# Performance work log

Hardware: AMD Instinct MI355X
Metric: run time of the kernel (lower is better)

## Reference

```python
import jax, jax.numpy as jnp
import numpy as np

B, S, HID = 2, 2048, 2048
H, G = 16, 1
D = HID // H  # 128


def setup_inputs() -> dict:
    key = jax.random.key(0)
    ks = jax.random.split(key, 10)
    sc = 0.02
    inp = {
        "hidden_states": jax.random.normal(ks[0], (B, S, HID), jnp.float32),
        # 1 above the diagonal -> masked out (matches torch code: scores += mask * -1e9)
        "causal_mask": jnp.triu(jnp.ones((1, 1, S, S), jnp.float32), k=1),
        "padding_mask": jnp.zeros((B, S), jnp.float32),
        "Wq": jax.random.normal(ks[1], (HID, HID), jnp.float32) * sc,
        "bq": jnp.zeros((HID,), jnp.float32),
        "Wk": jax.random.normal(ks[2], (G * D, HID), jnp.float32) * sc,
        "bk": jnp.zeros((G * D,), jnp.float32),
        "Wv": jax.random.normal(ks[3], (G * D, HID), jnp.float32) * sc,
        "bv": jnp.zeros((G * D,), jnp.float32),
        "Wo": jax.random.normal(ks[4], (HID, HID), jnp.float32) * sc,
        "bo": jnp.zeros((HID,), jnp.float32),
    }
    return inp


def reference(hidden_states, causal_mask, padding_mask, Wq, bq, Wk, bk, Wv, bv, Wo, bo):
    b, s, _ = hidden_states.shape
    q = hidden_states @ Wq.T + bq            # [B,S,HID]
    k = hidden_states @ Wk.T + bk            # [B,S,G*D]
    v = hidden_states @ Wv.T + bv            # [B,S,G*D]
    q = q.reshape(b, s, H, D).transpose(0, 2, 1, 3)   # [B,H,S,D]
    k = k.reshape(b, s, G, D).transpose(0, 2, 1, 3)   # [B,G,S,D]
    v = v.reshape(b, s, G, D).transpose(0, 2, 1, 3)   # [B,G,S,D]
    # broadcast G=1 KV heads against H query heads (exactly what torch.matmul does)
    scores = jnp.matmul(q, jnp.swapaxes(k, -1, -2)) / jnp.sqrt(jnp.float32(D))  # [B,H,S,S]
    scores = scores + causal_mask * (-1e9)
    scores = scores + padding_mask[:, None, None, :] * (-1e9)
    weights = jax.nn.softmax(scores, axis=-1)
    out = jnp.matmul(weights, v)                       # [B,H,S,D]
    out = out.transpose(0, 2, 1, 3).reshape(b, s, H * D)
    return out @ Wo.T + bo
```

## Files before the change

kernel.cpp:

```cpp
#include <hip/hip_runtime.h>
#include <hip/hip_bf16.h>

typedef __attribute__((ext_vector_type(8))) short s8v;
typedef __attribute__((ext_vector_type(4))) float f4v;
typedef __hip_bfloat16 bf16;

#define S_LEN 2048
#define HID_DIM 2048
#define N_HEADS 16
#define HEAD_D 128
#define M_ROWS 4096
#define N_FUSED 2304

#define EXP2F(x) __builtin_amdgcn_exp2f(x)

static __device__ inline short f2b_bits(float f) {
  bf16 h = __float2bfloat16(f);
  short u;
  __builtin_memcpy(&u, &h, 2);
  return u;
}
static __device__ inline unsigned pk_bf16(float a, float b) {
  __hip_bfloat162 h2 = __float22bfloat162_rn(float2{a, b});
  unsigned u;
  __builtin_memcpy(&u, &h2, 4);
  return u;
}

struct Cvt5 {
  const float* src[5];
  bf16* dst[5];
  long n8[5];
};

__global__ __launch_bounds__(256) void cvt_f32_bf16(Cvt5 c) {
  long i = (long)blockIdx.x * 256 + threadIdx.x;
#pragma unroll
  for (int s = 0; s < 5; ++s) {
    long n8 = c.n8[s];
    if (i < n8) {
      const float* p = c.src[s] + i * 8;
      float4 f0 = *(const float4*)p;
      float4 f1 = *(const float4*)(p + 4);
      s8v t;
      t[0] = f2b_bits(f0.x); t[1] = f2b_bits(f0.y);
      t[2] = f2b_bits(f0.z); t[3] = f2b_bits(f0.w);
      t[4] = f2b_bits(f1.x); t[5] = f2b_bits(f1.y);
      t[6] = f2b_bits(f1.z); t[7] = f2b_bits(f1.w);
      *(s8v*)(c.dst[s] + i * 8) = t;
      return;
    }
    i -= n8;
  }
}

__global__ __launch_bounds__(256) void gemm_qkv(
    const bf16* __restrict__ A, const bf16* __restrict__ Wf,
    const float* __restrict__ bq, const float* __restrict__ bk,
    const float* __restrict__ bv,
    bf16* __restrict__ qout, bf16* __restrict__ kout, bf16* __restrict__ vtout) {
  __shared__ __align__(16) bf16 As[128 * 72];
  __shared__ __align__(16) bf16 Bs[128 * 72];
  const int t = threadIdx.x;
  const int lane = t & 63, wid = t >> 6;
  const int l15 = lane & 15, quad = lane >> 4;
  const int wm = wid >> 1, wn = wid & 1;
  const int bm = blockIdx.x, bn = blockIdx.y;
  f4v acc[4][4] = {};
  for (int kt = 0; kt < HID_DIM / 64; ++kt) {
    __syncthreads();
#pragma unroll
    for (int i = 0; i < 4; ++i) {
      int idx = t + i * 256;
      int row = idx >> 3, c8 = (idx & 7) * 8;
      *(uint4*)&As[row * 72 + c8] =
          *(const uint4*)&A[(size_t)(bm * 128 + row) * HID_DIM + kt * 64 + c8];
      *(uint4*)&Bs[row * 72 + c8] =
          *(const uint4*)&Wf[(size_t)(bn * 128 + row) * HID_DIM + kt * 64 + c8];
    }
    __syncthreads();
#pragma unroll
    for (int ks = 0; ks < 2; ++ks) {
      s8v af[4], bfr[4];
#pragma unroll
      for (int mi = 0; mi < 4; ++mi)
        af[mi] = *(const s8v*)&As[(wm * 64 + mi * 16 + l15) * 72 + ks * 32 + quad * 8];
#pragma unroll
      for (int ni = 0; ni < 4; ++ni)
        bfr[ni] = *(const s8v*)&Bs[(wn * 64 + ni * 16 + l15) * 72 + ks * 32 + quad * 8];
#pragma unroll
      for (int mi = 0; mi < 4; ++mi)
#pragma unroll
        for (int ni = 0; ni < 4; ++ni)
          acc[mi][ni] = __builtin_amdgcn_mfma_f32_16x16x32_bf16(af[mi], bfr[ni], acc[mi][ni], 0, 0, 0);
    }
  }
  if (bn < 16) {
#pragma unroll
    for (int ni = 0; ni < 4; ++ni) {
      int cl = wn * 64 + ni * 16 + l15;
      float bvv = bq[bn * 128 + cl];
#pragma unroll
      for (int mi = 0; mi < 4; ++mi)
#pragma unroll
        for (int r = 0; r < 4; ++r) {
          int row = bm * 128 + wm * 64 + mi * 16 + quad * 4 + r;
          qout[(size_t)row * HID_DIM + bn * 128 + cl] = __float2bfloat16(acc[mi][ni][r] + bvv);
        }
    }
  } else if (bn == 16) {
#pragma unroll
    for (int ni = 0; ni < 4; ++ni) {
      int cl = wn * 64 + ni * 16 + l15;
      float bvv = bk[cl];
#pragma unroll
      for (int mi = 0; mi < 4; ++mi)
#pragma unroll
        for (int r = 0; r < 4; ++r) {
          int row = bm * 128 + wm * 64 + mi * 16 + quad * 4 + r;
          kout[(size_t)row * HEAD_D + cl] = __float2bfloat16(acc[mi][ni][r] + bvv);
        }
    }
  } else {
#pragma unroll
    for (int ni = 0; ni < 4; ++ni) {
      int cl = wn * 64 + ni * 16 + l15;
      float bvv = bv[cl];
#pragma unroll
      for (int mi = 0; mi < 4; ++mi)
#pragma unroll
        for (int r = 0; r < 4; ++r) {
          int row = bm * 128 + wm * 64 + mi * 16 + quad * 4 + r;
          vtout[(size_t)cl * M_ROWS + row] = __float2bfloat16(acc[mi][ni][r] + bvv);
        }
    }
  }
}

template <bool WBF>
__global__ __launch_bounds__(256) void gemm_o(
    const bf16* __restrict__ A, const void* __restrict__ Wp,
    const float* __restrict__ bias, float* __restrict__ C) {
  __shared__ __align__(16) bf16 As[128 * 72];
  __shared__ __align__(16) bf16 Bs[128 * 72];
  const int t = threadIdx.x;
  const int lane = t & 63, wid = t >> 6;
  const int l15 = lane & 15, quad = lane >> 4;
  const int wm = wid >> 1, wn = wid & 1;
  const int bm = blockIdx.x, bn = blockIdx.y;
  f4v acc[4][4] = {};
  for (int kt = 0; kt < HID_DIM / 64; ++kt) {
    __syncthreads();
#pragma unroll
    for (int i = 0; i < 4; ++i) {
      int idx = t + i * 256;
      int row = idx >> 3, c8 = (idx & 7) * 8;
      *(uint4*)&As[row * 72 + c8] =
          *(const uint4*)&A[(size_t)(bm * 128 + row) * HID_DIM + kt * 64 + c8];
      if constexpr (WBF) {
        *(uint4*)&Bs[row * 72 + c8] =
            *(const uint4*)&((const bf16*)Wp)[(size_t)(bn * 128 + row) * HID_DIM + kt * 64 + c8];
      } else {
        const float* s = (const float*)Wp + (size_t)(bn * 128 + row) * HID_DIM + kt * 64 + c8;
        float4 f0 = *(const float4*)s;
        float4 f1 = *(const float4*)(s + 4);
        s8v tmp;
        tmp[0] = f2b_bits(f0.x); tmp[1] = f2b_bits(f0.y);
        tmp[2] = f2b_bits(f0.z); tmp[3] = f2b_bits(f0.w);
        tmp[4] = f2b_bits(f1.x); tmp[5] = f2b_bits(f1.y);
        tmp[6] = f2b_bits(f1.z); tmp[7] = f2b_bits(f1.w);
        *(s8v*)&Bs[row * 72 + c8] = tmp;
      }
    }
    __syncthreads();
#pragma unroll
    for (int ks = 0; ks < 2; ++ks) {
      s8v af[4], bfr[4];
#pragma unroll
      for (int mi = 0; mi < 4; ++mi)
        af[mi] = *(const s8v*)&As[(wm * 64 + mi * 16 + l15) * 72 + ks * 32 + quad * 8];
#pragma unroll
      for (int ni = 0; ni < 4; ++ni)
        bfr[ni] = *(const s8v*)&Bs[(wn * 64 + ni * 16 + l15) * 72 + ks * 32 + quad * 8];
#pragma unroll
      for (int mi = 0; mi < 4; ++mi)
#pragma unroll
        for (int ni = 0; ni < 4; ++ni)
          acc[mi][ni] = __builtin_amdgcn_mfma_f32_16x16x32_bf16(af[mi], bfr[ni], acc[mi][ni], 0, 0, 0);
    }
  }
#pragma unroll
  for (int ni = 0; ni < 4; ++ni) {
    int col = bn * 128 + wn * 64 + ni * 16 + l15;
    float bvv = bias[col];
#pragma unroll
    for (int mi = 0; mi < 4; ++mi)
#pragma unroll
      for (int r = 0; r < 4; ++r) {
        int row = bm * 128 + wm * 64 + mi * 16 + quad * 4 + r;
        C[(size_t)row * HID_DIM + col] = acc[mi][ni][r] + bvv;
      }
  }
}

__global__ __launch_bounds__(256, 2) void attn_fwd(
    const bf16* q, const bf16* __restrict__ k, const bf16* __restrict__ vt,
    bf16* o) {
  constexpr int FS = 528;
  __shared__ __align__(16) bf16 KsF[16 * FS];
  __shared__ __align__(16) bf16 VtF[16 * FS];
  __shared__ __align__(16) bf16 PsF[16 * FS];
  const int t = threadIdx.x;
  const int lane = t & 63, w = t >> 6;
  const int l15 = lane & 15, quad = lane >> 4;
  const int u = blockIdx.x >> 1, b = blockIdx.x & 1;
  const int c = (u < 128) ? (255 - 2 * u) : (2 * (u - 128));
  const size_t bs = (size_t)b * S_LEN;
  const int row0 = c * 8;

  s8v qf[2][4];
#pragma unroll
  for (int mi = 0; mi < 2; ++mi)
#pragma unroll
    for (int ks = 0; ks < 4; ++ks)
      qf[mi][ks] = *(const s8v*)&q[(bs + row0 + (l15 & 7)) * HID_DIM +
                                   (w * 4 + mi * 2 + (l15 >> 3)) * HEAD_D + ks * 32 + quad * 8];

  float mst[2] = {-1e30f, -1e30f};
  float lst[2] = {0.f, 0.f};
  f4v acco[2][8] = {};
  const float scale2 = 0.12754245f;
  const int jt = (c >> 3) + 1;

  uint4 kreg[4], vreg[4];
#pragma unroll
  for (int i = 0; i < 4; ++i) {
    int idx = t + i * 256;
    kreg[i] = *(const uint4*)&k[(bs + (idx >> 4)) * HEAD_D + (idx & 15) * 8];
    vreg[i] = *(const uint4*)&vt[(size_t)(idx >> 3) * M_ROWS + bs + (idx & 7) * 8];
  }

  for (int j = 0; j < jt; ++j) {
    __syncthreads();
#pragma unroll
    for (int i = 0; i < 4; ++i) {
      int idx = t + i * 256;
      int krow = idx >> 4, kc = idx & 15;
      *(uint4*)&KsF[(((krow >> 4) << 2) | (kc >> 2)) * FS + ((krow & 15) << 5) + ((kc & 3) << 3)] = kreg[i];
      int vd = idx >> 3, vc = idx & 7;
      *(uint4*)&VtF[(((vd >> 4) << 1) | (vc >> 2)) * FS + ((vd & 15) << 5) + ((vc & 3) << 3)] = vreg[i];
    }
    if (j + 1 < jt) {
#pragma unroll
      for (int i = 0; i < 4; ++i) {
        int idx = t + i * 256;
        kreg[i] = *(const uint4*)&k[(bs + (j + 1) * 64 + (idx >> 4)) * HEAD_D + (idx & 15) * 8];
        vreg[i] = *(const uint4*)&vt[(size_t)(idx >> 3) * M_ROWS + bs + (j + 1) * 64 + (idx & 7) * 8];
      }
    }
    __syncthreads();

    f4v accs[4][2] = {};
#pragma unroll
    for (int ks = 0; ks < 4; ++ks) {
      s8v kf[4];
#pragma unroll
      for (int ni = 0; ni < 4; ++ni)
        kf[ni] = *(const s8v*)&KsF[(ni * 4 + ks) * FS + l15 * 32 + quad * 8];
#pragma unroll
      for (int ni = 0; ni < 4; ++ni)
#pragma unroll
        for (int mi = 0; mi < 2; ++mi)
          accs[ni][mi] = __builtin_amdgcn_mfma_f32_16x16x32_bf16(kf[ni], qf[mi][ks], accs[ni][mi], 0, 0, 0);
    }

#pragma unroll
    for (int mi = 0; mi < 2; ++mi) {
      const int mg = row0 + (l15 & 7);
      const bool full = (j * 64 + 63 <= row0);
      float tmax = -1e30f;
#pragma unroll
      for (int ni = 0; ni < 4; ++ni)
#pragma unroll
        for (int r = 0; r < 4; ++r) {
          int ng = j * 64 + ni * 16 + quad * 4 + r;
          float s = accs[ni][mi][r];
          if (!full && ng > mg) s = -1e30f;
          accs[ni][mi][r] = s;
          tmax = fmaxf(tmax, s);
        }
      tmax = fmaxf(tmax, __shfl_xor(tmax, 16, 64));
      tmax = fmaxf(tmax, __shfl_xor(tmax, 32, 64));
      float mnew = fmaxf(mst[mi], tmax);
      float nms = -mnew * scale2;
      float alpha = EXP2F(fmaf(mst[mi], scale2, nms));
      float psum = 0.f;
#pragma unroll
      for (int ni = 0; ni < 4; ++ni) {
        float p0 = EXP2F(fmaf(accs[ni][mi][0], scale2, nms));
        float p1 = EXP2F(fmaf(accs[ni][mi][1], scale2, nms));
        float p2 = EXP2F(fmaf(accs[ni][mi][2], scale2, nms));
        float p3 = EXP2F(fmaf(accs[ni][mi][3], scale2, nms));
        psum += (p0 + p1) + (p2 + p3);
        uint2 packed;
        packed.x = pk_bf16(p0, p1);
        packed.y = pk_bf16(p2, p3);
        *(uint2*)&PsF[(w * 4 + mi * 2 + (ni >> 1)) * FS + l15 * 32 + (ni & 1) * 16 + quad * 4] = packed;
      }
      psum += __shfl_xor(psum, 16, 64);
      psum += __shfl_xor(psum, 32, 64);
      lst[mi] = lst[mi] * alpha + psum;
      mst[mi] = mnew;
#pragma unroll
      for (int r = 0; r < 4; ++r) {
        float ar = __shfl(alpha, quad * 4 + r, 64);
#pragma unroll
        for (int di = 0; di < 8; ++di) acco[mi][di][r] *= ar;
      }
    }

#pragma unroll
    for (int ks = 0; ks < 2; ++ks) {
      s8v pf[2], vf[8];
#pragma unroll
      for (int mi = 0; mi < 2; ++mi)
        pf[mi] = *(const s8v*)&PsF[(w * 4 + mi * 2 + ks) * FS + l15 * 32 + quad * 8];
#pragma unroll
      for (int di = 0; di < 8; ++di)
        vf[di] = *(const s8v*)&VtF[(di * 2 + ks) * FS + l15 * 32 + quad * 8];
#pragma unroll
      for (int mi = 0; mi < 2; ++mi)
#pragma unroll
        for (int di = 0; di < 8; ++di)
          acco[mi][di] = __builtin_amdgcn_mfma_f32_16x16x32_bf16(pf[mi], vf[di], acco[mi][di], 0, 0, 0);
    }
  }

#pragma unroll
  for (int mi = 0; mi < 2; ++mi)
#pragma unroll
    for (int r = 0; r < 4; ++r) {
      int vmq = quad * 4 + r;
      float lr = __shfl(lst[mi], vmq, 64);
      float rinv = 1.0f / lr;
      size_t row = bs + row0 + (vmq & 7);
      int head = w * 4 + mi * 2 + (vmq >> 3);
#pragma unroll
      for (int di = 0; di < 8; ++di)
        o[row * HID_DIM + head * HEAD_D + di * 16 + l15] = __float2bfloat16(acco[mi][di][r] * rinv);
    }
}

extern "C" void kernel_launch(void* const* d_in, const int* in_sizes, int n_in,
                              void* d_out, int out_size, void* d_ws, size_t ws_size,
                              hipStream_t stream) {
  const float* hs = (const float*)d_in[0];
  const float* Wq = (const float*)d_in[3];
  const float* bq = (const float*)d_in[4];
  const float* Wk = (const float*)d_in[5];
  const float* bk = (const float*)d_in[6];
  const float* Wv = (const float*)d_in[7];
  const float* bv = (const float*)d_in[8];
  const float* Wo = (const float*)d_in[9];
  const float* bo = (const float*)d_in[10];
  float* out = (float*)d_out;

  bf16* qab = (bf16*)d_ws;
  const bool big_ws = ws_size >= (size_t)25 * 1024 * 1024;
  bf16* wob = (bf16*)((char*)d_ws + (size_t)16 * 1024 * 1024);

  char* ob = (char*)d_out;
  bf16* kb = (bf16*)ob;
  bf16* vtb = (bf16*)(ob + (size_t)1048576);
  bf16* hsb = (bf16*)(ob + (size_t)2097152);
  bf16* wqkvb = (bf16*)(ob + (size_t)18874368);

  Cvt5 c;
  c.src[0] = hs; c.dst[0] = hsb;
  c.n8[0] = (long)M_ROWS * HID_DIM / 8;
  c.src[1] = Wq; c.dst[1] = wqkvb;
  c.n8[1] = (long)HID_DIM * HID_DIM / 8;
  c.src[2] = Wk; c.dst[2] = wqkvb + (size_t)HID_DIM * HID_DIM;
  c.n8[2] = (long)HEAD_D * HID_DIM / 8;
  c.src[3] = Wv; c.dst[3] = wqkvb + (size_t)(HID_DIM + HEAD_D) * HID_DIM;
  c.n8[3] = (long)HEAD_D * HID_DIM / 8;
  c.src[4] = Wo; c.dst[4] = big_ws ? wob : (bf16*)nullptr;
  c.n8[4] = big_ws ? (long)HID_DIM * HID_DIM / 8 : 0;
  long total8 = c.n8[0] + c.n8[1] + c.n8[2] + c.n8[3] + c.n8[4];

  cvt_f32_bf16<<<dim3((unsigned)((total8 + 255) / 256)), dim3(256), 0, stream>>>(c);
  gemm_qkv<<<dim3(M_ROWS / 128, N_FUSED / 128), dim3(256), 0, stream>>>(
      hsb, wqkvb, bq, bk, bv, qab, kb, vtb);
  attn_fwd<<<dim3(512), dim3(256), 0, stream>>>(qab, kb, vtb, qab);
  if (big_ws)
    gemm_o<true><<<dim3(M_ROWS / 128, HID_DIM / 128), dim3(256), 0, stream>>>(qab, wob, bo, out);
  else
    gemm_o<false><<<dim3(M_ROWS / 128, HID_DIM / 128), dim3(256), 0, stream>>>(qab, Wo, bo, out);
}
```

Measured before the change: 424.8 us.

## Use 512-thread attention blocks, each processing a paired short and long query chunk

The attention kernel now launches 256 blocks of 8 waves instead of 512 blocks of 4 waves. Each block handles two causal row chunks, c = 255-p followed by c = p, so every block does a similar amount of work. Each wave now covers 2 heads with a single Q fragment set instead of 4 heads, which lowers register pressure. In exchange, every K and V fragment read from LDS feeds half as many MFMAs, and the tail balance now depends on one block per CU.

```diff
diff --git a/kernel.cpp b/kernel.cpp
--- a/kernel.cpp
+++ b/kernel.cpp
@@ -203,7 +203,7 @@
   }
 }
 
-__global__ __launch_bounds__(256, 2) void attn_fwd(
+__global__ __launch_bounds__(512, 2) void attn_fwd(
     const bf16* q, const bf16* __restrict__ k, const bf16* __restrict__ vt,
     bf16* o) {
   constexpr int FS = 528;
@@ -213,69 +213,66 @@
   const int t = threadIdx.x;
   const int lane = t & 63, w = t >> 6;
   const int l15 = lane & 15, quad = lane >> 4;
-  const int u = blockIdx.x >> 1, b = blockIdx.x & 1;
-  const int c = (u < 128) ? (255 - 2 * u) : (2 * (u - 128));
+  const int p = blockIdx.x >> 1, b = blockIdx.x & 1;
   const size_t bs = (size_t)b * S_LEN;
-  const int row0 = c * 8;
-
-  s8v qf[2][4];
-#pragma unroll
-  for (int mi = 0; mi < 2; ++mi)
+  const float scale2 = 0.12754245f;
+
+  for (int cc = 0; cc < 2; ++cc) {
+    const int c = cc ? p : (255 - p);
+    const int row0 = c * 8;
+    const int jt = (c >> 3) + 1;
+    const int head = w * 2 + (l15 >> 3);
+
+    s8v qf[4];
 #pragma unroll
     for (int ks = 0; ks < 4; ++ks)
-      qf[mi][ks] = *(const s8v*)&q[(bs + row0 + (l15 & 7)) * HID_DIM +
-                                   (w * 4 + mi * 2 + (l15 >> 3)) * HEAD_D + ks * 32 + quad * 8];
-
-  float mst[2] = {-1e30f, -1e30f};
-  float lst[2] = {0.f, 0.f};
-  f4v acco[2][8] = {};
-  const float scale2 = 0.12754245f;
-  const int jt = (c >> 3) + 1;
-
-  uint4 kreg[4], vreg[4];
-#pragma unroll
-  for (int i = 0; i < 4; ++i) {
-    int idx = t + i * 256;
-    kreg[i] = *(const uint4*)&k[(bs + (idx >> 4)) * HEAD_D + (idx & 15) * 8];
-    vreg[i] = *(const uint4*)&vt[(size_t)(idx >> 3) * M_ROWS + bs + (idx & 7) * 8];
-  }
-
-  for (int j = 0; j < jt; ++j) {
-    __syncthreads();
-#pragma unroll
-    for (int i = 0; i < 4; ++i) {
-      int idx = t + i * 256;
-      int krow = idx >> 4, kc = idx & 15;
-      *(uint4*)&KsF[(((krow >> 4) << 2) | (kc >> 2)) * FS + ((krow & 15) << 5) + ((kc & 3) << 3)] = kreg[i];
-      int vd = idx >> 3, vc = idx & 7;
-      *(uint4*)&VtF[(((vd >> 4) << 1) | (vc >> 2)) * FS + ((vd & 15) << 5) + ((vc & 3) << 3)] = vreg[i];
-    }
-    if (j + 1 < jt) {
-#pragma unroll
-      for (int i = 0; i < 4; ++i) {
-        int idx = t + i * 256;
-        kreg[i] = *(const uint4*)&k[(bs + (j + 1) * 64 + (idx >> 4)) * HEAD_D + (idx & 15) * 8];
-        vreg[i] = *(const uint4*)&vt[(size_t)(idx >> 3) * M_ROWS + bs + (j + 1) * 64 + (idx & 7) * 8];
-      }
-    }
-    __syncthreads();
-
-    f4v accs[4][2] = {};
-#pragma unroll
-    for (int ks = 0; ks < 4; ++ks) {
-      s8v kf[4];
-#pragma unroll
-      for (int ni = 0; ni < 4; ++ni)
-        kf[ni] = *(const s8v*)&KsF[(ni * 4 + ks) * FS + l15 * 32 + quad * 8];
-#pragma unroll
-      for (int ni = 0; ni < 4; ++ni)
-#pragma unroll
-        for (int mi = 0; mi < 2; ++mi)
-          accs[ni][mi] = __builtin_amdgcn_mfma_f32_16x16x32_bf16(kf[ni], qf[mi][ks], accs[ni][mi], 0, 0, 0);
-    }
-
-#pragma unroll
-    for (int mi = 0; mi < 2; ++mi) {
+      qf[ks] = *(const s8v*)&q[(bs + row0 + (l15 & 7)) * HID_DIM +
+                               head * HEAD_D + ks * 32 + quad * 8];
+
+    float mst = -1e30f;
+    float lst = 0.f;
+    f4v acco[8] = {};
+
+    uint4 kreg[2], vreg[2];
+#pragma unroll
+    for (int i = 0; i < 2; ++i) {
+      int idx = t + i * 512;
+      kreg[i] = *(const uint4*)&k[(bs + (idx >> 4)) * HEAD_D + (idx & 15) * 8];
+      vreg[i] = *(const uint4*)&vt[(size_t)(idx >> 3) * M_ROWS + bs + (idx & 7) * 8];
+    }
+
+    for (int j = 0; j < jt; ++j) {
+      __syncthreads();
+#pragma unroll
+      for (int i = 0; i < 2; ++i) {
+        int idx = t + i * 512;
+        int krow = idx >> 4, kc = idx & 15;
+        *(uint4*)&KsF[(((krow >> 4) << 2) | (kc >> 2)) * FS + ((krow & 15) << 5) + ((kc & 3) << 3)] = kreg[i];
+        int vd = idx >> 3, vc = idx & 7;
+        *(uint4*)&VtF[(((vd >> 4) << 1) | (vc >> 2)) * FS + ((vd & 15) << 5) + ((vc & 3) << 3)] = vreg[i];
+      }
+      if (j + 1 < jt) {
+#pragma unroll
+        for (int i = 0; i < 2; ++i) {
+          int idx = t + i * 512;
+          kreg[i] = *(const uint4*)&k[(bs + (j + 1) * 64 + (idx >> 4)) * HEAD_D + (idx & 15) * 8];
+          vreg[i] = *(const uint4*)&vt[(size_t)(idx >> 3) * M_ROWS + bs + (j + 1) * 64 + (idx & 7) * 8];
+        }
+      }
+      __syncthreads();
+
+      f4v accs[4] = {};
+#pragma unroll
+      for (int ks = 0; ks < 4; ++ks) {
+        s8v kf[4];
+#pragma unroll
+        for (int ni = 0; ni < 4; ++ni)
+          kf[ni] = *(const s8v*)&KsF[(ni * 4 + ks) * FS + l15 * 32 + quad * 8];
+#pragma unroll
+        for (int ni = 0; ni < 4; ++ni)
+          accs[ni] = __builtin_amdgcn_mfma_f32_16x16x32_bf16(kf[ni], qf[ks], accs[ni], 0, 0, 0);
+      }
+
       const int mg = row0 + (l15 & 7);
       const bool full = (j * 64 + 63 <= row0);
       float tmax = -1e30f;
@@ -284,71 +281,65 @@
 #pragma unroll
         for (int r = 0; r < 4; ++r) {
           int ng = j * 64 + ni * 16 + quad * 4 + r;
-          float s = accs[ni][mi][r];
+          float s = accs[ni][r];
           if (!full && ng > mg) s = -1e30f;
-          accs[ni][mi][r] = s;
+          accs[ni][r] = s;
           tmax = fmaxf(tmax, s);
         }
       tmax = fmaxf(tmax, __shfl_xor(tmax, 16, 64));
       tmax = fmaxf(tmax, __shfl_xor(tmax, 32, 64));
-      float mnew = fmaxf(mst[mi], tmax);
+      float mnew = fmaxf(mst, tmax);
       float nms = -mnew * scale2;
-      float alpha = EXP2F(fmaf(mst[mi], scale2, nms));
+      float alpha = EXP2F(fmaf(mst, scale2, nms));
       float psum = 0.f;
 #pragma unroll
       for (int ni = 0; ni < 4; ++ni) {
-        float p0 = EXP2F(fmaf(accs[ni][mi][0], scale2, nms));
-        float p1 = EXP2F(fmaf(accs[ni][mi][1], scale2, nms));
-        float p2 = EXP2F(fmaf(accs[ni][mi][2], scale2, nms));
-        float p3 = EXP2F(fmaf(accs[ni][mi][3], scale2, nms));
+        float p0 = EXP2F(fmaf(accs[ni][0], scale2, nms));
+        float p1 = EXP2F(fmaf(accs[ni][1], scale2, nms));
+        float p2 = EXP2F(fmaf(accs[ni][2], scale2, nms));
+        float p3 = EXP2F(fmaf(accs[ni][3], scale2, nms));
         psum += (p0 + p1) + (p2 + p3);
         uint2 packed;
         packed.x = pk_bf16(p0, p1);
         packed.y = pk_bf16(p2, p3);
-        *(uint2*)&PsF[(w * 4 + mi * 2 + (ni >> 1)) * FS + l15 * 32 + (ni & 1) * 16 + quad * 4] = packed;
+        *(uint2*)&PsF[(w * 2 + (ni >> 1)) * FS + l15 * 32 + (ni & 1) * 16 + quad * 4] = packed;
       }
       psum += __shfl_xor(psum, 16, 64);
       psum += __shfl_xor(psum, 32, 64);
-      lst[mi] = lst[mi] * alpha + psum;
-      mst[mi] = mnew;
+      lst = lst * alpha + psum;
+      mst = mnew;
 #pragma unroll
       for (int r = 0; r < 4; ++r) {
         float ar = __shfl(alpha, quad * 4 + r, 64);
 #pragma unroll
-        for (int di = 0; di < 8; ++di) acco[mi][di][r] *= ar;
-      }
-    }
-
-#pragma unroll
-    for (int ks = 0; ks < 2; ++ks) {
-      s8v pf[2], vf[8];
-#pragma unroll
-      for (int mi = 0; mi < 2; ++mi)
-        pf[mi] = *(const s8v*)&PsF[(w * 4 + mi * 2 + ks) * FS + l15 * 32 + quad * 8];
-#pragma unroll
-      for (int di = 0; di < 8; ++di)
-        vf[di] = *(const s8v*)&VtF[(di * 2 + ks) * FS + l15 * 32 + quad * 8];
-#pragma unroll
-      for (int mi = 0; mi < 2; ++mi)
+        for (int di = 0; di < 8; ++di) acco[di][r] *= ar;
+      }
+
+#pragma unroll
+      for (int ks = 0; ks < 2; ++ks) {
+        s8v pf, vf[8];
+        pf = *(const s8v*)&PsF[(w * 2 + ks) * FS + l15 * 32 + quad * 8];
 #pragma unroll
         for (int di = 0; di < 8; ++di)
-          acco[mi][di] = __builtin_amdgcn_mfma_f32_16x16x32_bf16(pf[mi], vf[di], acco[mi][di], 0, 0, 0);
-    }
-  }
-
-#pragma unroll
-  for (int mi = 0; mi < 2; ++mi)
+          vf[di] = *(const s8v*)&VtF[(di * 2 + ks) * FS + l15 * 32 + quad * 8];
+#pragma unroll
+        for (int di = 0; di < 8; ++di)
+          acco[di] = __builtin_amdgcn_mfma_f32_16x16x32_bf16(pf, vf[di], acco[di], 0, 0, 0);
+      }
+    }
+
 #pragma unroll
     for (int r = 0; r < 4; ++r) {
       int vmq = quad * 4 + r;
-      float lr = __shfl(lst[mi], vmq, 64);
+      float lr = __shfl(lst, vmq, 64);
       float rinv = 1.0f / lr;
       size_t row = bs + row0 + (vmq & 7);
-      int head = w * 4 + mi * 2 + (vmq >> 3);
+      int hd = w * 2 + (vmq >> 3);
 #pragma unroll
       for (int di = 0; di < 8; ++di)
-        o[row * HID_DIM + head * HEAD_D + di * 16 + l15] = __float2bfloat16(acco[mi][di][r] * rinv);
-    }
+        o[row * HID_DIM + hd * HEAD_D + di * 16 + l15] = __float2bfloat16(acco[di][r] * rinv);
+    }
+  }
 }
 
 extern "C" void kernel_launch(void* const* d_in, const int* in_sizes, int n_in,
@@ -391,7 +382,7 @@
   cvt_f32_bf16<<<dim3((unsigned)((total8 + 255) / 256)), dim3(256), 0, stream>>>(c);
   gemm_qkv<<<dim3(M_ROWS / 128, N_FUSED / 128), dim3(256), 0, stream>>>(
       hsb, wqkvb, bq, bk, bv, qab, kb, vtb);
-  attn_fwd<<<dim3(512), dim3(256), 0, stream>>>(qab, kb, vtb, qab);
+  attn_fwd<<<dim3(256), dim3(512), 0, stream>>>(qab, kb, vtb, qab);
   if (big_ws)
     gemm_o<true><<<dim3(M_ROWS / 128, HID_DIM / 128), dim3(256), 0, stream>>>(qab, wob, bo, out);
   else
```

Result: faster. 387.3 us (-8.8%).
